# Optimization experiments

Hardware: AMD Instinct MI355X
Metric: run time of the kernel (lower is better)

## Reference

```python
import jax, jax.numpy as jnp
import numpy as np

D_MODEL = 176

def setup_inputs() -> dict:
    key = jax.random.key(0)
    x = jax.random.normal(key, (8192, D_MODEL), dtype=jnp.float32)
    return {"x": x}

def reference(x) -> jnp.ndarray:
    # Original torch loop computes, per batch item i: x[i] * eye(d) -> diag matrix
    # with x[i] on the diagonal, then cats along batch. Vectorized: diag-embed.
    b, d = x.shape
    eye = jnp.eye(d, dtype=x.dtype)            # [d, d]
    embed = x[:, None, :] * eye[None, :, :]    # [b, d, d]; nonzero only at (j, j)
    return embed
```

## Files before the change

kernel.cpp:

```cpp
#include <hip/hip_runtime.h>


#define D_MODEL 176
#define ROW_VEC (D_MODEL / 4)

typedef float fvec4 __attribute__((ext_vector_type(4)));

__global__ __launch_bounds__(256) void diag_embed_kernel(
    const float* __restrict__ x,
    fvec4* __restrict__ out,
    unsigned int total_vec) {
    unsigned int idx = blockIdx.x * 256u + threadIdx.x;
    if (idx >= total_vec) return;

    unsigned int row = idx / ROW_VEC;
    unsigned int pos = idx - row * ROW_VEC;
    unsigned int j   = row % D_MODEL;
    unsigned int i   = row / D_MODEL;

    fvec4 v = (fvec4)(0.f, 0.f, 0.f, 0.f);
    unsigned int c0 = pos * 4u;
    unsigned int off = j - c0;
    if (off < 4u) {
        float val = x[i * D_MODEL + j];
        v[off] = val;
    }
    __builtin_nontemporal_store(v, &out[idx]);
}

extern "C" void kernel_launch(void* const* d_in, const int* in_sizes, int n_in,
                              void* d_out, int out_size, void* d_ws, size_t ws_size,
                              hipStream_t stream) {
    const float* x = (const float*)d_in[0];
    fvec4* out = (fvec4*)d_out;

    unsigned int total_vec = (unsigned int)(out_size / 4);
    unsigned int grid = (total_vec + 255u) / 256u;

    diag_embed_kernel<<<grid, 256, 0, stream>>>(x, out, total_vec);
}
```

Baseline: 989.8 us.

## Zero output with memset and scatter diagonal values in a separate kernel

```diff
diff --git a/kernel.cpp b/kernel.cpp
--- a/kernel.cpp
+++ b/kernel.cpp
@@ -2,40 +2,29 @@
 
 
 #define D_MODEL 176
-#define ROW_VEC (D_MODEL / 4)
 
-typedef float fvec4 __attribute__((ext_vector_type(4)));
+__global__ __launch_bounds__(256) void diag_scatter_kernel(
+    const float* __restrict__ x,
+    float* __restrict__ out,
+    unsigned int n) {
+    unsigned int t = blockIdx.x * 256u + threadIdx.x;
+    if (t >= n) return;
 
-__global__ __launch_bounds__(256) void diag_embed_kernel(
-    const float* __restrict__ x,
-    fvec4* __restrict__ out,
-    unsigned int total_vec) {
-    unsigned int idx = blockIdx.x * 256u + threadIdx.x;
-    if (idx >= total_vec) return;
-
-    unsigned int row = idx / ROW_VEC;
-    unsigned int pos = idx - row * ROW_VEC;
-    unsigned int j   = row % D_MODEL;
-    unsigned int i   = row / D_MODEL;
-
-    fvec4 v = (fvec4)(0.f, 0.f, 0.f, 0.f);
-    unsigned int c0 = pos * 4u;
-    unsigned int off = j - c0;
-    if (off < 4u) {
-        float val = x[i * D_MODEL + j];
-        v[off] = val;
-    }
-    __builtin_nontemporal_store(v, &out[idx]);
+    float val = x[t];
+    unsigned int i = t / D_MODEL;
+    unsigned int j = t - i * D_MODEL;
+    out[i * (D_MODEL * D_MODEL) + j * (D_MODEL + 1)] = val;
 }
 
 extern "C" void kernel_launch(void* const* d_in, const int* in_sizes, int n_in,
                               void* d_out, int out_size, void* d_ws, size_t ws_size,
                               hipStream_t stream) {
     const float* x = (const float*)d_in[0];
-    fvec4* out = (fvec4*)d_out;
+    float* out = (float*)d_out;
 
-    unsigned int total_vec = (unsigned int)(out_size / 4);
-    unsigned int grid = (total_vec + 255u) / 256u;
+    hipMemsetAsync(d_out, 0, (size_t)out_size * sizeof(float), stream);
 
-    diag_embed_kernel<<<grid, 256, 0, stream>>>(x, out, total_vec);
+    unsigned int n = (unsigned int)in_sizes[0];
+    unsigned int grid = (n + 255u) / 256u;
+    diag_scatter_kernel<<<grid, 256, 0, stream>>>(x, out, n);
 }
```

After: 1.067 ms. +7.8%, slower.
